# Kernel optimization log

Hardware: AMD Instinct MI355X
Metric: run time of the kernel (lower is better)

## Reference

```python
import jax, jax.numpy as jnp
from jax import lax
import numpy as np

H = W = 224
N = H * W
T = 25          # landscape sample points
K_MAX = 2       # number of landscapes
M_PTS = 64      # max persistence-diagram points kept (top persistence)
OUT_F = 50
CHUNK = 512     # pixels per DTM chunk


def _make_offsets(m0):
    # static, sorted-by-distance local window covering >= m0 fraction of mass for near-uniform weights
    r = int(np.ceil(np.sqrt(m0 * N / np.pi) * 1.3))
    dy, dx = np.meshgrid(np.arange(-r, r + 1), np.arange(-r, r + 1), indexing="ij")
    d2 = (dy * dy + dx * dx).astype(np.float32).ravel()
    o = np.argsort(d2, kind="stable")
    return jnp.asarray(dy.ravel()[o]), jnp.asarray(dx.ravel()[o]), jnp.asarray(d2[o]), r

_OFF = {m0: _make_offsets(m0) for m0 in (0.05, 0.2)}


def _dtm(w_img, m0):
    """Weighted distance-to-measure on the unit-spacing 224x224 grid.
    dtm(x)^2 = (1/(m0*W)) * sum of w_j * d_j^2 over nearest grid points until cumulative
    weight reaches m0*W (partial weight on the crossing point). Offsets are pre-sorted by
    distance (identical for every pixel), so no per-pixel sort is needed."""
    dy, dx, d2, r = _OFF[m0]
    B = w_img.shape[0]
    wp = jnp.pad(w_img, ((0, 0), (r, r), (r, r)))
    thr = m0 * w_img.sum(axis=(1, 2))                      # (B,)
    pix = jnp.arange(N).reshape(N // CHUNK, CHUNK)

    def body(p):
        y = p // W + r
        x = p % W + r
        vals = wp[:, y[:, None] + dy[None, :], x[:, None] + dx[None, :]]  # (B,C,O)
        c = jnp.cumsum(vals, axis=-1)
        used = jnp.minimum(jnp.maximum(thr[:, None, None] - (c - vals), 0.0), vals)
        return jnp.einsum("bco,o->bc", used, d2) / thr[:, None]

    dtm2 = lax.map(jax.checkpoint(body), pix)              # (n_chunks, B, CHUNK)
    return jnp.sqrt(jnp.maximum(dtm2.transpose(1, 0, 2).reshape(B, N), 0.0))


def _h0_pairs_np(f_batch):
    """0-dim persistent homology (sublevel filtration, 4-connectivity) via union-find.
    Returns indices of birth/death pixels so birth/death VALUES can be gathered
    differentiably in jax (PLLay-style gradients)."""
    f_batch = np.asarray(f_batch)
    B = f_batch.shape[0]
    b_idx = np.zeros((B, M_PTS), np.int32)
    d_idx = np.zeros((B, M_PTS), np.int32)
    mask = np.zeros((B, M_PTS), np.bool_)
    for bb in range(B):
        f = f_batch[bb]
        order = np.argsort(f, kind="stable")
        parent = np.full(N, -1, np.int64)
        pairs = []
        for i in order:
            i = int(i)
            parent[i] = i
            y, x = divmod(i, W)
            nbs = []
            if y > 0: nbs.append(i - W)
            if y < H - 1: nbs.append(i + W)
            if x > 0: nbs.append(i - 1)
            if x < W - 1: nbs.append(i + 1)
            for nb in nbs:
                if parent[nb] < 0:
                    continue
                ri = i
                while parent[ri] != ri:
                    parent[ri] = parent[parent[ri]]; ri = parent[ri]
                rn = nb
                while parent[rn] != rn:
                    parent[rn] = parent[parent[rn]]; rn = parent[rn]
                if ri == rn:
                    continue
                if f[ri] <= f[rn]:
                    elder, young = ri, rn
                else:
                    elder, young = rn, ri
                pairs.append((young, i))   # elder rule: younger component dies here
                parent[young] = elder
        pairs.append((int(np.argmin(f)), int(np.argmax(f))))  # essential class
        pa = np.asarray(pairs, np.int64)
        pers = f[pa[:, 1]] - f[pa[:, 0]]
        keep = np.argsort(-pers)[:M_PTS]
        k = len(keep)
        b_idx[bb, :k] = pa[keep, 0]
        d_idx[bb, :k] = pa[keep, 1]
        mask[bb, :k] = pers[keep] > 0
    return b_idx, d_idx, mask


def _topo_layer(x_img, m0, tseq, gw, gb):
    # AdTopoLayer: DTM -> H0 persistence diagram -> persistence landscapes at tseq -> Linear
    dt = _dtm(x_img, m0)                                   # (B, N)
    B = dt.shape[0]
    shapes = (jax.ShapeDtypeStruct((B, M_PTS), np.int32),
              jax.ShapeDtypeStruct((B, M_PTS), np.int32),
              jax.ShapeDtypeStruct((B, M_PTS), np.bool_))
    b_idx, d_idx, mask = jax.pure_callback(_h0_pairs_np, shapes, lax.stop_gradient(dt))
    birth = jnp.take_along_axis(dt, b_idx, axis=1)         # differentiable gather
    death = jnp.take_along_axis(dt, d_idx, axis=1)
    death = jnp.where(mask, death, birth)                  # invalid slots -> zero tent
    t = tseq[None, None, :]                                # (1,1,T)
    tents = jnp.maximum(jnp.minimum(t - birth[:, :, None], death[:, :, None] - t), 0.0)
    lam, _ = lax.top_k(tents.transpose(0, 2, 1), K_MAX)    # (B,T,K): k-th largest tents
    feat = lam.transpose(0, 2, 1).reshape(B, K_MAX * T)    # (B,50)
    return feat @ gw.T + gb


def _forward(input, params):
    xs = []
    for m0, g in ((0.05, "1"), (0.2, "2")):
        for c in range(3):
            n = "t" + g + str(c + 1)
            xs.append(_topo_layer(input[:, c], m0, params[n + "_tseq"], params[n + "_w"], params[n + "_b"]))
    x = jnp.concatenate(xs, axis=-1)                       # (B, 300)
    signal = jnp.abs(lax.stop_gradient(x)).sum(axis=0)     # (300,) detached signal
    output = jax.nn.relu(x) @ params["fc_w"].T + params["fc_b"]
    return output, signal


def setup_inputs():
    key = jax.random.key(0)
    ks = jax.random.split(key, 8)
    B = 2
    inp = {"input": jax.random.uniform(ks[0], (B, 3, H, W), jnp.float32)}
    centers = {"1": 20.0, "2": 40.0}   # typical DTM value ranges for m0=0.05 / 0.2
    i = 1
    for g in ("1", "2"):
        for c in ("1", "2", "3"):
            n = "t" + g + c
            kk = jax.random.fold_in(ks[1], i)
            inp[n + "_tseq"] = jnp.linspace(centers[g] - 15.0, centers[g] + 15.0, T).astype(jnp.float32)
            inp[n + "_w"] = 0.1 * jax.random.normal(kk, (OUT_F, K_MAX * T), jnp.float32)
            inp[n + "_b"] = jnp.zeros((OUT_F,), jnp.float32)
            i += 1
    inp["fc_w"] = 0.1 * jax.random.normal(ks[2], (7, 6 * OUT_F), jnp.float32)
    inp["fc_b"] = jnp.zeros((7,), jnp.float32)
    return inp


def reference(input, t11_tseq, t11_w, t11_b, t12_tseq, t12_w, t12_b, t13_tseq, t13_w, t13_b, t21_tseq, t21_w, t21_b, t22_tseq, t22_w, t22_b, t23_tseq, t23_w, t23_b, fc_w, fc_b):
    params = dict(t11_tseq=t11_tseq, t11_w=t11_w, t11_b=t11_b,
                  t12_tseq=t12_tseq, t12_w=t12_w, t12_b=t12_b,
                  t13_tseq=t13_tseq, t13_w=t13_w, t13_b=t13_b,
                  t21_tseq=t21_tseq, t21_w=t21_w, t21_b=t21_b,
                  t22_tseq=t22_tseq, t22_w=t22_w, t22_b=t22_b,
                  t23_tseq=t23_tseq, t23_w=t23_w, t23_b=t23_b,
                  fc_w=fc_w, fc_b=fc_b)
    return _forward(input, params)
```

## Files before the change

### kernel.cpp

```cpp
#include <hip/hip_runtime.h>
#include <stdint.h>

#define HWDIM 224
#define NPIX (HWDIM*HWDIM)
#define NFIELD 12
#define TT 25

#define R1v 37
#define PW1v (HWDIM + 2*R1v)
#define R2v 74
#define PW2v (HWDIM + 2*R2v)

#define HSIZE 16384
#define FCAP 4096
#define RHASH 4096
#define DON 36

typedef unsigned long long u64;

struct LayerParams {
    const float* tseq[6];
    const float* gw[6];
    const float* gb[6];
};

constexpr size_t alup(size_t x) { return (x + 255) & ~(size_t)255; }
constexpr size_t SZPA = (size_t)6*PW1v*(PW1v+1)*4;
constexpr size_t SZPB = (size_t)6*PW2v*(PW2v+1)*4;
constexpr size_t OFF_SUMS = 0;
constexpr size_t OFF_P0A = alup(OFF_SUMS + 8*4);
constexpr size_t OFF_PZA = alup(OFF_P0A + SZPA);
constexpr size_t OFF_P0B = alup(OFF_PZA + 2*SZPA);
constexpr size_t OFF_PZB = alup(OFF_P0B + SZPB);
constexpr size_t OFF_DT   = alup(OFF_PZB + 2*SZPB);
constexpr size_t OFF_PAR  = alup(OFF_DT   + (size_t)NFIELD*NPIX*4);
constexpr size_t OFF_HP   = alup(OFF_PAR  + (size_t)NFIELD*NPIX*2);
constexpr size_t OFF_HB   = alup(OFF_HP   + (size_t)NFIELD*HSIZE*8);
constexpr size_t OFF_GMM  = OFF_HB + (size_t)NFIELD*HSIZE*8;
constexpr size_t OFF_X    = alup(OFF_GMM + 256);


__global__ __launch_bounds__(64) void k_prefix(const float* __restrict__ inp,
        float* __restrict__ p0a, float2* __restrict__ pza,
        float* __restrict__ p0b, float2* __restrict__ pzb) {
    int bidx = blockIdx.x;
    const int tot0 = 6 * PW1v;
    int g = (bidx >= tot0);
    int rem = g ? (bidx - tot0) : bidx;
    const int PW = g ? PW2v : PW1v, R = g ? R2v : R1v, C = PW + 1;
    int img = rem / PW, row = rem % PW;
    float* P0 = (g ? p0b : p0a) + ((size_t)img*PW + row) * C;
    float2* PZ = (g ? pzb : pza) + ((size_t)img*PW + row) * C;
    int iy = row - R;
    bool rowok = ((unsigned)iy < HWDIM);
    const float* src = inp + (size_t)img*NPIX + (size_t)(rowok ? iy : 0)*HWDIM;
    const int lane = threadIdx.x;
    if (lane == 0) { P0[0] = 0.f; PZ[0] = make_float2(0.f, 0.f); }
    float c0 = 0.f, c1 = 0.f, c2 = 0.f;
    for (int i = 0; i < 6; ++i) {
        int k = i*64 + lane;
        float v = 0.f;
        if (k < PW && rowok) { int ix = k - R; if ((unsigned)ix < HWDIM) v = src[ix]; }
        float xd = (float)k;
        float w0 = v, w1 = v*xd, w2 = v*xd*xd;
        #pragma unroll
        for (int off = 1; off < 64; off <<= 1) {
            float t0 = __shfl_up(w0, off), t1 = __shfl_up(w1, off), t2 = __shfl_up(w2, off);
            if (lane >= off) { w0 += t0; w1 += t1; w2 += t2; }
        }
        if (k < PW) {
            P0[k+1] = c0 + w0;
            PZ[k+1] = make_float2(c1 + w1, c2 + w2);
        }
        c0 += __shfl(w0, 63); c1 += __shfl(w1, 63); c2 += __shfl(w2, 63);
    }
}

__global__ __launch_bounds__(256) void k_sums2(const float* __restrict__ p0a,
        float* __restrict__ sums) {
    int img = blockIdx.x;
    __shared__ float red[256];
    float s = 0.f;
    const int C = PW1v + 1;
    for (int r = threadIdx.x; r < PW1v; r += 256)
        s += p0a[((size_t)img*PW1v + r)*C + PW1v];
    red[threadIdx.x] = s; __syncthreads();
    for (int w = 128; w > 0; w >>= 1) {
        if (threadIdx.x < w) red[threadIdx.x] += red[threadIdx.x + w];
        __syncthreads();
    }
    if (threadIdx.x == 0) sums[img] = red[0];
}

__device__ __forceinline__ int k_init_exact(int X, int R) {
    int K = (int)sqrtf((float)X) + 1;
    if (K > R) K = R;
    while (K > 0 && K*K > X) --K;
    return K;
}

__device__ __forceinline__ float dmass1(int X, const float* __restrict__ P0, int bidx,
        int C, int R) {
    float m = 0.f;
    int K = 0;
    if (X >= 0) {
        K = k_init_exact(X, R);
        m = P0[bidx+K+1] - P0[bidx-K];
    }
    int t = X - 1, step = 3;
    const float* __restrict__ Pu = P0 - C;
    const float* __restrict__ Pd = P0 + C;
    for (int dyy = 1; dyy <= R; ++dyy) {
        if (__all(t < 0)) break;
        if (t >= 0) {
            while (K*K > t) --K;
            int A = bidx + K + 1, B = bidx - K;
            m += (Pu[A] - Pu[B]) + (Pd[A] - Pd[B]);
        }
        t -= step; step += 2; Pu -= C; Pd += C;
    }
    return m;
}

__global__ __launch_bounds__(256) void k_dtm(const float* __restrict__ sums,
        const float* __restrict__ p0a, const float2* __restrict__ pza,
        const float* __restrict__ p0b, const float2* __restrict__ pzb,
        float* __restrict__ dt) {
    const int xcd = blockIdx.x & 7, slot = blockIdx.x >> 3;
    int f, blk;
    if (xcd < 6) {
        if (slot < 196)            { f = 6 + xcd; blk = slot; }
        else if (slot < 196 + DON) { f = xcd; blk = (196 - DON) + (slot - 196); }
        else return;
    } else {
        const int per = 196 - DON;
        if (slot >= 3*per) return;
        int q = slot / per;
        f = (xcd - 6)*3 + q; blk = slot - q*per;
    }
    const int layer = f >> 1, b = f & 1;
    const int g = layer / 3, c = layer % 3;
    const int img = b*3 + c;
    const int R = g ? R2v : R1v, PW = g ? PW2v : PW1v, C = PW + 1;
    const int R2 = 2*R*R;
    const float thr = (g ? 0.2f : 0.05f) * sums[img];
    const float* __restrict__ P0 = (g ? p0b : p0a) + (size_t)img*PW*C;
    const float2* __restrict__ PZ = (g ? pzb : pza) + (size_t)img*PW*C;

    const int p = blk*256 + threadIdx.x;
    const int y = p / HWDIM, x = p % HWDIM;
    const int xc = x + R;
    const int bidx = (y + R)*C + xc;

    const int NP = g ? 7 : 6;
    const int WSTOP = g ? 86 : 43;
    int lo = 0, hi = R2 + 1;
    for (int it = 0; it < NP; ++it) {
        int X = (lo + hi) >> 1;
        float m = dmass1(X, P0, bidx, C, R);
        if (m >= thr) hi = X; else lo = X + 1;
    }
    for (int rit = 0; rit < 14; ++rit) {
        bool act = (hi == R2 + 1) ? (lo < hi) : (hi - lo > WSTOP);
        if (__all(!act)) break;
        int X = act ? ((lo + hi) >> 1) : -1;
        float m = dmass1(X, P0, bidx, C, R);
        if (X >= 0) { if (m >= thr) hi = X; else lo = X + 1; }
    }
    const bool nr = (hi == R2 + 1);
    const int  Dst = nr ? lo : ((lo + hi) >> 1);
    const bool cross = nr ? (lo <= R2) : true;
    const int  Xin = cross ? (Dst - 1) : R2;

    float m_in = 0.f, ws = 0.f;
    const float c2n = -2.f * (float)xc;
    const int xc2i = xc * xc;
    int K = 0;
    if (Xin >= 0) {
        K = k_init_exact(Xin, R);
        int A = bidx+K+1, B = bidx-K;
        float s0 = P0[A] - P0[B]; float2 zA = PZ[A], zB = PZ[B];
        m_in += s0; ws += fmaf((float)xc2i, s0, fmaf(c2n, zA.x - zB.x, zA.y - zB.y));
    }
    {
        int t = Xin - 1, step = 3, d2 = 1;
        const float* __restrict__ Pu = P0 - C;
        const float* __restrict__ Pd = P0 + C;
        const float2* __restrict__ Zu = PZ - C;
        const float2* __restrict__ Zd = PZ + C;
        for (int dyy = 1; dyy <= R; ++dyy) {
            if (__all(t < 0)) break;
            if (t >= 0) {
                while (K*K > t) --K;
                int A = bidx+K+1, B = bidx-K;
                float c1 = (float)(d2 + xc2i);
                { float s0 = Pu[A]-Pu[B]; float2 zA = Zu[A], zB = Zu[B];
                  m_in += s0; ws += fmaf(c1, s0, fmaf(c2n, zA.x - zB.x, zA.y - zB.y)); }
                { float s0 = Pd[A]-Pd[B]; float2 zA = Zd[A], zB = Zd[B];
                  m_in += s0; ws += fmaf(c1, s0, fmaf(c2n, zA.x - zB.x, zA.y - zB.y)); }
            }
            t -= step; d2 += step; step += 2;
            Pu -= C; Pd += C; Zu -= C; Zd += C;
        }
    }
    float s = cross ? (ws + (float)Dst * (thr - m_in)) : ws;
    float d = sqrtf(fmaxf(s / thr, 0.f));
    dt[(size_t)f*NPIX + p] = d;
}

__global__ __launch_bounds__(256) void k_desc(const float* __restrict__ dt,
        unsigned short* __restrict__ par, u64* __restrict__ gmm) {
    const int f = blockIdx.y;
    const int p = blockIdx.x*256 + threadIdx.x;
    const float* __restrict__ dtf = dt + (size_t)f*NPIX;
    float dc = dtf[p];
    u64 kc = ((u64)__float_as_uint(dc) << 32) | (unsigned)p;
    u64 best = kc; int bi = p;
    const int y = p / HWDIM, x = p % HWDIM;
    if (y > 0)        { float v = dtf[p - HWDIM]; u64 t = ((u64)__float_as_uint(v)<<32)|(unsigned)(p-HWDIM); if (t < best) { best = t; bi = p-HWDIM; } }
    if (y < HWDIM-1)  { float v = dtf[p + HWDIM]; u64 t = ((u64)__float_as_uint(v)<<32)|(unsigned)(p+HWDIM); if (t < best) { best = t; bi = p+HWDIM; } }
    if (x > 0)        { float v = dtf[p - 1];     u64 t = ((u64)__float_as_uint(v)<<32)|(unsigned)(p-1);     if (t < best) { best = t; bi = p-1; } }
    if (x < HWDIM-1)  { float v = dtf[p + 1];     u64 t = ((u64)__float_as_uint(v)<<32)|(unsigned)(p+1);     if (t < best) { best = t; bi = p+1; } }
    par[(size_t)f*NPIX + p] = (unsigned short)bi;
    __shared__ u64 rmin[256], rmax[256];
    u64 mk = ((u64)__float_as_uint(dc) << 32) | (unsigned)(0xFFFF - p);
    rmin[threadIdx.x] = kc; rmax[threadIdx.x] = mk;
    __syncthreads();
    for (int w = 128; w > 0; w >>= 1) {
        if (threadIdx.x < w) {
            if (rmin[threadIdx.x + w] < rmin[threadIdx.x]) rmin[threadIdx.x] = rmin[threadIdx.x + w];
            if (rmax[threadIdx.x + w] > rmax[threadIdx.x]) rmax[threadIdx.x] = rmax[threadIdx.x + w];
        }
        __syncthreads();
    }
    if (threadIdx.x == 0) {
        atomicMin(&gmm[f*2 + 0], rmin[0]);
        atomicMin(&gmm[f*2 + 1], ~rmax[0]);
    }
}

__device__ inline unsigned hash64(u64 x) {
    x ^= x >> 33; x *= 0xff51afd7ed558ccdULL;
    x ^= x >> 33; x *= 0xc4ceb9fe1a85ec53ULL;
    x ^= x >> 33;
    return (unsigned)x;
}

struct FinSh {
    u64 ek[FCAP];
    unsigned int epk[FCAP];
    unsigned int eab[FCAP];
    unsigned short eru[FCAP];
    int rhk[RHASH];
    short ufp[RHASH];
    float rdt[RHASH];
    unsigned int pyd[FCAP];
    float ppr[FCAP];
};

__device__ __forceinline__ void bitonic_n(u64* ek, int tid, int n, int bst) {
    for (int k = 2; k <= n; k <<= 1) {
        for (int j = k >> 1; j > 0; j >>= 1) {
            for (int i = tid; i < n; i += bst) {
                int ixj = i ^ j;
                if (ixj > i) {
                    u64 a = ek[i], b = ek[ixj];
                    if (((i & k) == 0) ? (a > b) : (a < b)) { ek[i] = b; ek[ixj] = a; }
                }
            }
            __syncthreads();
        }
    }
}

__global__ __launch_bounds__(1024) void k_fused(const float* __restrict__ dt,
        const unsigned short* __restrict__ parg, const u64* __restrict__ gmm,
        u64* __restrict__ hpair, u64* __restrict__ hbest,
        LayerParams lp, float* __restrict__ xbuf) {
    const int xcd = blockIdx.x & 7, slot = blockIdx.x >> 3;
    int f;
    if (xcd < 6) { if (slot != 0) return; f = 6 + xcd; }
    else f = (xcd - 6)*3 + slot;
    const int layer = f >> 1, bb = f & 1;
    const int tid = threadIdx.x; const int bs = 1024;
    const float* dtf = dt + (size_t)f*NPIX;
    u64* hp = hpair + (size_t)f*HSIZE;
    u64* hb = hbest + (size_t)f*HSIZE;

    __shared__ union U {
        unsigned short par[NPIX];
        FinSh fin;
    } sh;
    __shared__ float birth[64], death[64], featsh[2*TT];
    __shared__ int spec_a[64], spec_b[64];
    __shared__ u64 spec_e[64];
    __shared__ int cnt_s, pc_s;
    __shared__ int gmin_s, gmax_s; __shared__ float gminf_s, gmaxf_s;

    {
        const unsigned* src = (const unsigned*)(parg + (size_t)f*NPIX);
        unsigned* dst = (unsigned*)sh.par;
        for (int i = tid; i < NPIX/2; i += bs) dst[i] = src[i];
    }
    if (tid == 0) {
        u64 g0v = gmm[f*2 + 0];
        u64 g1v = ~gmm[f*2 + 1];
        gmin_s = (int)(unsigned)(g0v & 0xFFFFFFFFu);
        gminf_s = __uint_as_float((unsigned)(g0v >> 32));
        gmax_s = 0xFFFF - (int)(g1v & 0xFFFFu);
        gmaxf_s = __uint_as_float((unsigned)(g1v >> 32));
        cnt_s = 0; pc_s = 0;
    }
    __syncthreads();
    for (int pass = 0; pass < 6; ++pass) {
        for (int p = tid; p < NPIX; p += bs) sh.par[p] = sh.par[sh.par[p]];
        __syncthreads();
    }
    for (int p = tid; p < NPIX; p += bs) {
        int a = sh.par[p];
        int n = sh.par[a];
        while (n != a) { a = n; n = sh.par[a]; }
        sh.par[p] = (unsigned short)a;
    }
    __syncthreads();
    for (int p = tid; p < NPIX; p += bs) {
        const int rp = sh.par[p];
        const int y = p / HWDIM, x = p % HWDIM;
        const float dp = dtf[p];
        #pragma unroll
        for (int e = 0; e < 2; ++e) {
            int q;
            if (e == 0) { if (x >= HWDIM-1) continue; q = p + 1; }
            else        { if (y >= HWDIM-1) continue; q = p + HWDIM; }
            int rq = sh.par[q];
            if (rq == rp) continue;
            float dq = dtf[q];
            bool pdies = (dp > dq) || (dp == dq && p > q);
            u64 ekv = pdies
                ? (((u64)__float_as_uint(dp) << 32) | ((u64)(unsigned)p << 16) | (unsigned)rp)
                : (((u64)__float_as_uint(dq) << 32) | ((u64)(unsigned)q << 16) | (unsigned)rq);
            int ra = min(rp, rq), rb = max(rp, rq);
            u64 pk = ((u64)(unsigned)ra << 32) | (unsigned)rb;
            unsigned h = hash64(pk) & (HSIZE - 1);
            for (int probe = 0; probe < HSIZE; ++probe) {
                u64 old = atomicCAS(&hp[h], ~0ull, pk);
                if (old == ~0ull || old == pk) { atomicMin(&hb[h], ekv); break; }
                h = (h + 1) & (HSIZE - 1);
            }
        }
    }
    __syncthreads();
    for (int i = tid; i < RHASH; i += bs) sh.fin.rhk[i] = -1;
    __syncthreads();
    for (int i = tid; i < HSIZE; i += bs) {
        u64 pk = hp[i];
        if (pk != ~0ull) {
            int slot2 = atomicAdd(&cnt_s, 1);
            if (slot2 < FCAP) {
                u64 e = hb[i];
                unsigned u = (unsigned)((e >> 16) & 0xFFFFu);
                unsigned ru = (unsigned)(e & 0xFFFFu);
                sh.fin.ek[slot2] = (e & 0xFFFFFFFF00000000ull) | ((u64)u << 16) | (unsigned)slot2;
                int ra = (int)(pk >> 32), rb = (int)(pk & 0xFFFFFFFFu);
                sh.fin.epk[slot2] = ((unsigned)ra << 16) | (unsigned)rb;
                sh.fin.eru[slot2] = (unsigned short)ru;
                #pragma unroll
                for (int pass = 0; pass < 2; ++pass) {
                    int r = pass ? rb : ra;
                    unsigned h = ((unsigned)r * 2654435761u) & (RHASH - 1);
                    for (int pr = 0; pr < RHASH; ++pr) {
                        int old = atomicCAS(&sh.fin.rhk[h], -1, r);
                        if (old == -1 || old == r) break;
                        h = (h + 1) & (RHASH - 1);
                    }
                }
            }
        }
    }
    __syncthreads();
    int cnt = min(cnt_s, FCAP);
    int n1 = 64; while (n1 < cnt) n1 <<= 1;
    for (int s2 = tid; s2 < cnt; s2 += bs) {
        unsigned pk2 = sh.fin.epk[s2];
        int ra = (int)(pk2 >> 16), rb = (int)(pk2 & 0xFFFFu);
        int ru = sh.fin.eru[s2];
        int rv = (ru == ra) ? rb : ra;
        int su = -1, sv = -1;
        { unsigned h = ((unsigned)ru * 2654435761u) & (RHASH - 1);
          for (int pr = 0; pr < RHASH; ++pr) { int v = sh.fin.rhk[h]; if (v == ru) { su = (int)h; break; } if (v == -1) break; h = (h + 1) & (RHASH - 1); } }
        { unsigned h = ((unsigned)rv * 2654435761u) & (RHASH - 1);
          for (int pr = 0; pr < RHASH; ++pr) { int v = sh.fin.rhk[h]; if (v == rv) { sv = (int)h; break; } if (v == -1) break; h = (h + 1) & (RHASH - 1); } }
        sh.fin.eab[s2] = ((unsigned)su << 16) | (unsigned)(sv & 0xFFFF);
    }
    for (int i = cnt + tid; i < n1; i += bs) sh.fin.ek[i] = ~0ull;
    for (int s2 = tid; s2 < RHASH; s2 += bs) {
        sh.fin.ufp[s2] = (short)s2;
        int r = sh.fin.rhk[s2];
        sh.fin.rdt[s2] = (r >= 0) ? dtf[r] : 0.f;
    }
    __syncthreads();

    bitonic_n(sh.fin.ek, tid, n1, bs);

    if (tid < 64) {
        int pc = 0;
        for (int base = 0; base < cnt; base += 64) {
            int i = base + tid;
            int sa = -1, sb = -1; u64 e = ~0ull;
            if (i < cnt) {
                e = sh.fin.ek[i];
                int idx = (int)(e & 0xFFFFu);
                unsigned ab = sh.fin.eab[idx];
                sa = (int)(ab >> 16); sb = (int)(ab & 0xFFFFu);
                if (sa != 0xFFFF && sb != 0xFFFF) {
                    while (sh.fin.ufp[sa] != sa) { short g2 = sh.fin.ufp[sh.fin.ufp[sa]]; sh.fin.ufp[sa] = g2; sa = g2; }
                    while (sh.fin.ufp[sb] != sb) { short g2 = sh.fin.ufp[sh.fin.ufp[sb]]; sh.fin.ufp[sb] = g2; sb = g2; }
                    if (sa == sb) sa = -1;
                } else { sa = -1; }
            }
            spec_a[tid] = sa; spec_b[tid] = sb; spec_e[tid] = e;
            if (tid == 0) {
                int lim = min(64, cnt - base);
                for (int j = 0; j < lim; ++j) {
                    int sa2 = spec_a[j];
                    if (sa2 < 0) continue;
                    int sb2 = spec_b[j];
                    u64 e2 = spec_e[j];
                    while (sh.fin.ufp[sa2] != sa2) { short g2 = sh.fin.ufp[sh.fin.ufp[sa2]]; sh.fin.ufp[sa2] = g2; sa2 = g2; }
                    while (sh.fin.ufp[sb2] != sb2) { short g2 = sh.fin.ufp[sh.fin.ufp[sb2]]; sh.fin.ufp[sb2] = g2; sb2 = g2; }
                    if (sa2 == sb2) continue;
                    float fa = sh.fin.rdt[sa2], fb = sh.fin.rdt[sb2];
                    int elder, young;
                    if (fa <= fb) { elder = sa2; young = sb2; } else { elder = sb2; young = sa2; }
                    sh.fin.ufp[young] = (short)elder;
                    float pers = __uint_as_float((unsigned)(e2 >> 32)) - sh.fin.rdt[young];
                    if (pers > 0.f && pc < FCAP - 1) {
                        int u = (int)((e2 >> 16) & 0xFFFFu);
                        sh.fin.pyd[pc] = ((unsigned)sh.fin.rhk[young] << 16) | (unsigned)u;
                        sh.fin.ppr[pc] = pers; ++pc;
                    }
                }
            }
        }
        if (tid == 0) {
            sh.fin.pyd[pc] = ((unsigned)gmin_s << 16) | (unsigned)gmax_s;
            sh.fin.ppr[pc] = gmaxf_s - gminf_s; ++pc;
            pc_s = pc;
        }
    }
    __syncthreads();
    const int pc = pc_s;
    int n2 = 64; while (n2 < pc) n2 <<= 1;

    for (int i = tid; i < n2; i += bs) {
        if (i < pc && sh.fin.ppr[i] > 0.f)
            sh.fin.ek[i] = ((u64)(0xFFFFFFFFu - __float_as_uint(sh.fin.ppr[i])) << 32) | (unsigned)i;
        else sh.fin.ek[i] = ~0ull;
    }
    __syncthreads();
    bitonic_n(sh.fin.ek, tid, n2, bs);
    if (tid < 64) {
        u64 e = sh.fin.ek[tid];
        int bpix = 0, dpix = 0, msk = 0;
        if (e != ~0ull) {
            int i = (int)(e & 0xFFFFFFFFu);
            unsigned pd2 = sh.fin.pyd[i];
            bpix = (int)(pd2 >> 16); dpix = (int)(pd2 & 0xFFFFu); msk = 1;
        }
        float bv = dtf[bpix];
        float dv = msk ? dtf[dpix] : bv;
        birth[tid] = bv; death[tid] = dv;
    }
    __syncthreads();
    if (tid < TT) {
        float t = lp.tseq[layer][tid];
        float m1 = 0.f, m2 = 0.f;
        for (int m = 0; m < 64; ++m) {
            float v = fmaxf(fminf(t - birth[m], death[m] - t), 0.f);
            if (v > m1) { m2 = m1; m1 = v; } else if (v > m2) m2 = v;
        }
        featsh[tid] = m1; featsh[TT + tid] = m2;
    }
    __syncthreads();
    if (tid < 50) {
        const float* w = lp.gw[layer] + tid * 50;
        float acc = lp.gb[layer][tid];
        #pragma unroll
        for (int j = 0; j < 50; ++j) acc = fmaf(featsh[j], w[j], acc);
        xbuf[bb*300 + layer*50 + tid] = acc;
    }
}

__global__ __launch_bounds__(512) void k_final(const float* __restrict__ x, const float* __restrict__ fcw,
        const float* __restrict__ fcb, float* __restrict__ out) {
    __shared__ float rl[2][300];
    const int tid = threadIdx.x;
    if (tid < 300) {
        float a0 = x[tid], a1 = x[300 + tid];
        out[14 + tid] = fabsf(a0) + fabsf(a1);
        rl[0][tid] = fmaxf(a0, 0.f);
        rl[1][tid] = fmaxf(a1, 0.f);
    }
    __syncthreads();
    if (tid < 14) {
        int b = tid / 7, i = tid % 7;
        float acc = fcb[i];
        const float* w = fcw + i * 300;
        for (int j = 0; j < 300; ++j) acc = fmaf(rl[b][j], w[j], acc);
        out[b*7 + i] = acc;
    }
}

extern "C" void kernel_launch(void* const* d_in, const int* in_sizes, int n_in,
                              void* d_out, int out_size, void* d_ws, size_t ws_size,
                              hipStream_t stream) {
    (void)in_sizes; (void)n_in; (void)out_size; (void)ws_size;
    const float* inp = (const float*)d_in[0];
    LayerParams lp;
    for (int l = 0; l < 6; ++l) {
        lp.tseq[l] = (const float*)d_in[1 + 3*l];
        lp.gw[l]   = (const float*)d_in[2 + 3*l];
        lp.gb[l]   = (const float*)d_in[3 + 3*l];
    }
    const float* fcw = (const float*)d_in[19];
    const float* fcb = (const float*)d_in[20];

    char* w = (char*)d_ws;
    float* sums = (float*)(w + OFF_SUMS);
    float* p0a = (float*)(w + OFF_P0A);
    float2* pza = (float2*)(w + OFF_PZA);
    float* p0b = (float*)(w + OFF_P0B);
    float2* pzb = (float2*)(w + OFF_PZB);
    float* dt = (float*)(w + OFF_DT);
    unsigned short* par = (unsigned short*)(w + OFF_PAR);
    u64* hp = (u64*)(w + OFF_HP);
    u64* hb = (u64*)(w + OFF_HB);
    u64* gmm = (u64*)(w + OFF_GMM);
    float* xbuf = (float*)(w + OFF_X);

    const int prefRows = 6*PW1v + 6*PW2v;
    hipLaunchKernelGGL(k_prefix, dim3(prefRows), dim3(64), 0, stream,
                       inp, p0a, pza, p0b, pzb);
    hipLaunchKernelGGL(k_sums2, dim3(6), dim3(256), 0, stream, p0a, sums);
    hipMemsetAsync(hp, 0xFF, (size_t)2*NFIELD*HSIZE*8 + 256, stream);
    const int maxslot = 3 * (196 - DON);
    hipLaunchKernelGGL(k_dtm, dim3(8 * maxslot), dim3(256), 0, stream,
                       sums, p0a, pza, p0b, pzb, dt);
    hipLaunchKernelGGL(k_desc, dim3(NPIX/256, NFIELD), dim3(256), 0, stream, dt, par, gmm);
    hipLaunchKernelGGL(k_fused, dim3(24), dim3(1024), 0, stream,
                       dt, par, gmm, hp, hb, lp, xbuf);
    hipLaunchKernelGGL(k_final, dim3(1), dim3(512), 0, stream, xbuf, fcw, fcb, (float*)d_out);
}
```

Before: 721.7 us.

## Split fused persistence kernel into root, edge and finish kernels; shrink DTM blocks

The single 12-block fused kernel is split in three: root compression (one block per field), edge hashing across a full grid of 256-thread blocks, and a finish kernel that consumes the hash tables. This spreads the global-atomic edge phase over many CUs instead of 12 blocks. The DTM kernel also moves to 64-thread blocks with rescaled XCD slot mapping for finer load balance. The cost is extra kernel launches and a global round-trip of the root array.

```diff
diff --git a/kernel.cpp b/kernel.cpp
--- a/kernel.cpp
+++ b/kernel.cpp
@@ -14,7 +14,8 @@
 #define HSIZE 16384
 #define FCAP 4096
 #define RHASH 4096
-#define DON 36
+#define DON64 144
+#define BPF 784
 
 typedef unsigned long long u64;
 
@@ -122,18 +123,18 @@
     return m;
 }
 
-__global__ __launch_bounds__(256) void k_dtm(const float* __restrict__ sums,
+__global__ __launch_bounds__(64) void k_dtm(const float* __restrict__ sums,
         const float* __restrict__ p0a, const float2* __restrict__ pza,
         const float* __restrict__ p0b, const float2* __restrict__ pzb,
         float* __restrict__ dt) {
     const int xcd = blockIdx.x & 7, slot = blockIdx.x >> 3;
     int f, blk;
     if (xcd < 6) {
-        if (slot < 196)            { f = 6 + xcd; blk = slot; }
-        else if (slot < 196 + DON) { f = xcd; blk = (196 - DON) + (slot - 196); }
+        if (slot < BPF)              { f = 6 + xcd; blk = slot; }
+        else if (slot < BPF + DON64) { f = xcd; blk = slot - DON64; }
         else return;
     } else {
-        const int per = 196 - DON;
+        const int per = BPF - DON64;
         if (slot >= 3*per) return;
         int q = slot / per;
         f = (xcd - 6)*3 + q; blk = slot - q*per;
@@ -147,7 +148,7 @@
     const float* __restrict__ P0 = (g ? p0b : p0a) + (size_t)img*PW*C;
     const float2* __restrict__ PZ = (g ? pzb : pza) + (size_t)img*PW*C;
 
-    const int p = blk*256 + threadIdx.x;
+    const int p = blk*64 + threadIdx.x;
     const int y = p / HWDIM, x = p % HWDIM;
     const int xc = x + R;
     const int bidx = (y + R)*C + xc;
@@ -239,6 +240,34 @@
     }
 }
 
+__global__ __launch_bounds__(1024) void k_root(unsigned short* __restrict__ parg) {
+    const int f = blockIdx.x;
+    const int tid = threadIdx.x; const int bs = 1024;
+    __shared__ unsigned short par[NPIX];
+    {
+        const unsigned* src = (const unsigned*)(parg + (size_t)f*NPIX);
+        unsigned* dst = (unsigned*)par;
+        for (int i = tid; i < NPIX/2; i += bs) dst[i] = src[i];
+    }
+    __syncthreads();
+    for (int pass = 0; pass < 6; ++pass) {
+        for (int p = tid; p < NPIX; p += bs) par[p] = par[par[p]];
+        __syncthreads();
+    }
+    for (int p = tid; p < NPIX; p += bs) {
+        int a = par[p];
+        int n = par[a];
+        while (n != a) { a = n; n = par[a]; }
+        par[p] = (unsigned short)a;
+    }
+    __syncthreads();
+    {
+        const unsigned* src = (const unsigned*)par;
+        unsigned* dst = (unsigned*)(parg + (size_t)f*NPIX);
+        for (int i = tid; i < NPIX/2; i += bs) dst[i] = src[i];
+    }
+}
+
 __device__ inline unsigned hash64(u64 x) {
     x ^= x >> 33; x *= 0xff51afd7ed558ccdULL;
     x ^= x >> 33; x *= 0xc4ceb9fe1a85ec53ULL;
@@ -246,17 +275,40 @@
     return (unsigned)x;
 }
 
-struct FinSh {
-    u64 ek[FCAP];
-    unsigned int epk[FCAP];
-    unsigned int eab[FCAP];
-    unsigned short eru[FCAP];
-    int rhk[RHASH];
-    short ufp[RHASH];
-    float rdt[RHASH];
-    unsigned int pyd[FCAP];
-    float ppr[FCAP];
-};
+__global__ __launch_bounds__(256) void k_edges(const float* __restrict__ dt,
+        const unsigned short* __restrict__ parg,
+        u64* __restrict__ hpair, u64* __restrict__ hbest) {
+    const int f = blockIdx.y;
+    const int p = blockIdx.x*256 + threadIdx.x;
+    const float* __restrict__ dtf = dt + (size_t)f*NPIX;
+    const unsigned short* __restrict__ par = parg + (size_t)f*NPIX;
+    u64* hp = hpair + (size_t)f*HSIZE;
+    u64* hb = hbest + (size_t)f*HSIZE;
+    const int rp = par[p];
+    const int y = p / HWDIM, x = p % HWDIM;
+    const float dp = dtf[p];
+    #pragma unroll
+    for (int e = 0; e < 2; ++e) {
+        int q;
+        if (e == 0) { if (x >= HWDIM-1) continue; q = p + 1; }
+        else        { if (y >= HWDIM-1) continue; q = p + HWDIM; }
+        int rq = par[q];
+        if (rq == rp) continue;
+        float dq = dtf[q];
+        bool pdies = (dp > dq) || (dp == dq && p > q);
+        u64 ekv = pdies
+            ? (((u64)__float_as_uint(dp) << 32) | ((u64)(unsigned)p << 16) | (unsigned)rp)
+            : (((u64)__float_as_uint(dq) << 32) | ((u64)(unsigned)q << 16) | (unsigned)rq);
+        int ra = min(rp, rq), rb = max(rp, rq);
+        u64 pk = ((u64)(unsigned)ra << 32) | (unsigned)rb;
+        unsigned h = hash64(pk) & (HSIZE - 1);
+        for (int probe = 0; probe < HSIZE; ++probe) {
+            u64 old = atomicCAS(&hp[h], ~0ull, pk);
+            if (old == ~0ull || old == pk) { atomicMin(&hb[h], ekv); break; }
+            h = (h + 1) & (HSIZE - 1);
+        }
+    }
+}
 
 __device__ __forceinline__ void bitonic_n(u64* ek, int tid, int n, int bst) {
     for (int k = 2; k <= n; k <<= 1) {
@@ -273,35 +325,32 @@
     }
 }
 
-__global__ __launch_bounds__(1024) void k_fused(const float* __restrict__ dt,
-        const unsigned short* __restrict__ parg, const u64* __restrict__ gmm,
-        u64* __restrict__ hpair, u64* __restrict__ hbest,
+__global__ __launch_bounds__(1024) void k_finish(const float* __restrict__ dt,
+        const u64* __restrict__ gmm,
+        const u64* __restrict__ hpair, const u64* __restrict__ hbest,
         LayerParams lp, float* __restrict__ xbuf) {
-    const int xcd = blockIdx.x & 7, slot = blockIdx.x >> 3;
-    int f;
-    if (xcd < 6) { if (slot != 0) return; f = 6 + xcd; }
-    else f = (xcd - 6)*3 + slot;
+    const int f = blockIdx.x;
     const int layer = f >> 1, bb = f & 1;
     const int tid = threadIdx.x; const int bs = 1024;
     const float* dtf = dt + (size_t)f*NPIX;
-    u64* hp = hpair + (size_t)f*HSIZE;
-    u64* hb = hbest + (size_t)f*HSIZE;
-
-    __shared__ union U {
-        unsigned short par[NPIX];
-        FinSh fin;
-    } sh;
+    const u64* hp = hpair + (size_t)f*HSIZE;
+    const u64* hb = hbest + (size_t)f*HSIZE;
+
+    __shared__ u64 ek[FCAP];
+    __shared__ unsigned int epk[FCAP];
+    __shared__ unsigned int eab[FCAP];
+    __shared__ unsigned short eru[FCAP];
+    __shared__ int rhk[RHASH];
+    __shared__ short ufp[RHASH];
+    __shared__ float rdt[RHASH];
+    __shared__ unsigned int pyd[FCAP];
+    __shared__ float ppr[FCAP];
     __shared__ float birth[64], death[64], featsh[2*TT];
     __shared__ int spec_a[64], spec_b[64];
     __shared__ u64 spec_e[64];
     __shared__ int cnt_s, pc_s;
     __shared__ int gmin_s, gmax_s; __shared__ float gminf_s, gmaxf_s;
 
-    {
-        const unsigned* src = (const unsigned*)(parg + (size_t)f*NPIX);
-        unsigned* dst = (unsigned*)sh.par;
-        for (int i = tid; i < NPIX/2; i += bs) dst[i] = src[i];
-    }
     if (tid == 0) {
         u64 g0v = gmm[f*2 + 0];
         u64 g1v = ~gmm[f*2 + 1];
@@ -311,46 +360,7 @@
         gmaxf_s = __uint_as_float((unsigned)(g1v >> 32));
         cnt_s = 0; pc_s = 0;
     }
-    __syncthreads();
-    for (int pass = 0; pass < 6; ++pass) {
-        for (int p = tid; p < NPIX; p += bs) sh.par[p] = sh.par[sh.par[p]];
-        __syncthreads();
-    }
-    for (int p = tid; p < NPIX; p += bs) {
-        int a = sh.par[p];
-        int n = sh.par[a];
-        while (n != a) { a = n; n = sh.par[a]; }
-        sh.par[p] = (unsigned short)a;
-    }
-    __syncthreads();
-    for (int p = tid; p < NPIX; p += bs) {
-        const int rp = sh.par[p];
-        const int y = p / HWDIM, x = p % HWDIM;
-        const float dp = dtf[p];
-        #pragma unroll
-        for (int e = 0; e < 2; ++e) {
-            int q;
-            if (e == 0) { if (x >= HWDIM-1) continue; q = p + 1; }
-            else        { if (y >= HWDIM-1) continue; q = p + HWDIM; }
-            int rq = sh.par[q];
-            if (rq == rp) continue;
-            float dq = dtf[q];
-            bool pdies = (dp > dq) || (dp == dq && p > q);
-            u64 ekv = pdies
-                ? (((u64)__float_as_uint(dp) << 32) | ((u64)(unsigned)p << 16) | (unsigned)rp)
-                : (((u64)__float_as_uint(dq) << 32) | ((u64)(unsigned)q << 16) | (unsigned)rq);
-            int ra = min(rp, rq), rb = max(rp, rq);
-            u64 pk = ((u64)(unsigned)ra << 32) | (unsigned)rb;
-            unsigned h = hash64(pk) & (HSIZE - 1);
-            for (int probe = 0; probe < HSIZE; ++probe) {
-                u64 old = atomicCAS(&hp[h], ~0ull, pk);
-                if (old == ~0ull || old == pk) { atomicMin(&hb[h], ekv); break; }
-                h = (h + 1) & (HSIZE - 1);
-            }
-        }
-    }
-    __syncthreads();
-    for (int i = tid; i < RHASH; i += bs) sh.fin.rhk[i] = -1;
+    for (int i = tid; i < RHASH; i += bs) rhk[i] = -1;
     __syncthreads();
     for (int i = tid; i < HSIZE; i += bs) {
         u64 pk = hp[i];
@@ -360,16 +370,16 @@
                 u64 e = hb[i];
                 unsigned u = (unsigned)((e >> 16) & 0xFFFFu);
                 unsigned ru = (unsigned)(e & 0xFFFFu);
-                sh.fin.ek[slot2] = (e & 0xFFFFFFFF00000000ull) | ((u64)u << 16) | (unsigned)slot2;
+                ek[slot2] = (e & 0xFFFFFFFF00000000ull) | ((u64)u << 16) | (unsigned)slot2;
                 int ra = (int)(pk >> 32), rb = (int)(pk & 0xFFFFFFFFu);
-                sh.fin.epk[slot2] = ((unsigned)ra << 16) | (unsigned)rb;
-                sh.fin.eru[slot2] = (unsigned short)ru;
+                epk[slot2] = ((unsigned)ra << 16) | (unsigned)rb;
+                eru[slot2] = (unsigned short)ru;
                 #pragma unroll
                 for (int pass = 0; pass < 2; ++pass) {
                     int r = pass ? rb : ra;
                     unsigned h = ((unsigned)r * 2654435761u) & (RHASH - 1);
                     for (int pr = 0; pr < RHASH; ++pr) {
-                        int old = atomicCAS(&sh.fin.rhk[h], -1, r);
+                        int old = atomicCAS(&rhk[h], -1, r);
                         if (old == -1 || old == r) break;
                         h = (h + 1) & (RHASH - 1);
                     }
@@ -381,26 +391,26 @@
     int cnt = min(cnt_s, FCAP);
     int n1 = 64; while (n1 < cnt) n1 <<= 1;
     for (int s2 = tid; s2 < cnt; s2 += bs) {
-        unsigned pk2 = sh.fin.epk[s2];
+        unsigned pk2 = epk[s2];
         int ra = (int)(pk2 >> 16), rb = (int)(pk2 & 0xFFFFu);
-        int ru = sh.fin.eru[s2];
+        int ru = eru[s2];
         int rv = (ru == ra) ? rb : ra;
         int su = -1, sv = -1;
         { unsigned h = ((unsigned)ru * 2654435761u) & (RHASH - 1);
-          for (int pr = 0; pr < RHASH; ++pr) { int v = sh.fin.rhk[h]; if (v == ru) { su = (int)h; break; } if (v == -1) break; h = (h + 1) & (RHASH - 1); } }
+          for (int pr = 0; pr < RHASH; ++pr) { int v = rhk[h]; if (v == ru) { su = (int)h; break; } if (v == -1) break; h = (h + 1) & (RHASH - 1); } }
         { unsigned h = ((unsigned)rv * 2654435761u) & (RHASH - 1);
-          for (int pr = 0; pr < RHASH; ++pr) { int v = sh.fin.rhk[h]; if (v == rv) { sv = (int)h; break; } if (v == -1) break; h = (h + 1) & (RHASH - 1); } }
-        sh.fin.eab[s2] = ((unsigned)su << 16) | (unsigned)(sv & 0xFFFF);
-    }
-    for (int i = cnt + tid; i < n1; i += bs) sh.fin.ek[i] = ~0ull;
+          for (int pr = 0; pr < RHASH; ++pr) { int v = rhk[h]; if (v == rv) { sv = (int)h; break; } if (v == -1) break; h = (h + 1) & (RHASH - 1); } }
+        eab[s2] = ((unsigned)su << 16) | (unsigned)(sv & 0xFFFF);
+    }
+    for (int i = cnt + tid; i < n1; i += bs) ek[i] = ~0ull;
     for (int s2 = tid; s2 < RHASH; s2 += bs) {
-        sh.fin.ufp[s2] = (short)s2;
-        int r = sh.fin.rhk[s2];
-        sh.fin.rdt[s2] = (r >= 0) ? dtf[r] : 0.f;
-    }
-    __syncthreads();
-
-    bitonic_n(sh.fin.ek, tid, n1, bs);
+        ufp[s2] = (short)s2;
+        int r = rhk[s2];
+        rdt[s2] = (r >= 0) ? dtf[r] : 0.f;
+    }
+    __syncthreads();
+
+    bitonic_n(ek, tid, n1, bs);
 
     if (tid < 64) {
         int pc = 0;
@@ -408,13 +418,13 @@
             int i = base + tid;
             int sa = -1, sb = -1; u64 e = ~0ull;
             if (i < cnt) {
-                e = sh.fin.ek[i];
+                e = ek[i];
                 int idx = (int)(e & 0xFFFFu);
-                unsigned ab = sh.fin.eab[idx];
+                unsigned ab = eab[idx];
                 sa = (int)(ab >> 16); sb = (int)(ab & 0xFFFFu);
                 if (sa != 0xFFFF && sb != 0xFFFF) {
-                    while (sh.fin.ufp[sa] != sa) { short g2 = sh.fin.ufp[sh.fin.ufp[sa]]; sh.fin.ufp[sa] = g2; sa = g2; }
-                    while (sh.fin.ufp[sb] != sb) { short g2 = sh.fin.ufp[sh.fin.ufp[sb]]; sh.fin.ufp[sb] = g2; sb = g2; }
+                    while (ufp[sa] != sa) { short g2 = ufp[ufp[sa]]; ufp[sa] = g2; sa = g2; }
+                    while (ufp[sb] != sb) { short g2 = ufp[ufp[sb]]; ufp[sb] = g2; sb = g2; }
                     if (sa == sb) sa = -1;
                 } else { sa = -1; }
             }
@@ -426,25 +436,25 @@
                     if (sa2 < 0) continue;
                     int sb2 = spec_b[j];
                     u64 e2 = spec_e[j];
-                    while (sh.fin.ufp[sa2] != sa2) { short g2 = sh.fin.ufp[sh.fin.ufp[sa2]]; sh.fin.ufp[sa2] = g2; sa2 = g2; }
-                    while (sh.fin.ufp[sb2] != sb2) { short g2 = sh.fin.ufp[sh.fin.ufp[sb2]]; sh.fin.ufp[sb2] = g2; sb2 = g2; }
+                    while (ufp[sa2] != sa2) { short g2 = ufp[ufp[sa2]]; ufp[sa2] = g2; sa2 = g2; }
+                    while (ufp[sb2] != sb2) { short g2 = ufp[ufp[sb2]]; ufp[sb2] = g2; sb2 = g2; }
                     if (sa2 == sb2) continue;
-                    float fa = sh.fin.rdt[sa2], fb = sh.fin.rdt[sb2];
+                    float fa = rdt[sa2], fb = rdt[sb2];
                     int elder, young;
                     if (fa <= fb) { elder = sa2; young = sb2; } else { elder = sb2; young = sa2; }
-                    sh.fin.ufp[young] = (short)elder;
-                    float pers = __uint_as_float((unsigned)(e2 >> 32)) - sh.fin.rdt[young];
+                    ufp[young] = (short)elder;
+                    float pers = __uint_as_float((unsigned)(e2 >> 32)) - rdt[young];
                     if (pers > 0.f && pc < FCAP - 1) {
                         int u = (int)((e2 >> 16) & 0xFFFFu);
-                        sh.fin.pyd[pc] = ((unsigned)sh.fin.rhk[young] << 16) | (unsigned)u;
-                        sh.fin.ppr[pc] = pers; ++pc;
+                        pyd[pc] = ((unsigned)rhk[young] << 16) | (unsigned)u;
+                        ppr[pc] = pers; ++pc;
                     }
                 }
             }
         }
         if (tid == 0) {
-            sh.fin.pyd[pc] = ((unsigned)gmin_s << 16) | (unsigned)gmax_s;
-            sh.fin.ppr[pc] = gmaxf_s - gminf_s; ++pc;
+            pyd[pc] = ((unsigned)gmin_s << 16) | (unsigned)gmax_s;
+            ppr[pc] = gmaxf_s - gminf_s; ++pc;
             pc_s = pc;
         }
     }
@@ -453,18 +463,18 @@
     int n2 = 64; while (n2 < pc) n2 <<= 1;
 
     for (int i = tid; i < n2; i += bs) {
-        if (i < pc && sh.fin.ppr[i] > 0.f)
-            sh.fin.ek[i] = ((u64)(0xFFFFFFFFu - __float_as_uint(sh.fin.ppr[i])) << 32) | (unsigned)i;
-        else sh.fin.ek[i] = ~0ull;
-    }
-    __syncthreads();
-    bitonic_n(sh.fin.ek, tid, n2, bs);
+        if (i < pc && ppr[i] > 0.f)
+            ek[i] = ((u64)(0xFFFFFFFFu - __float_as_uint(ppr[i])) << 32) | (unsigned)i;
+        else ek[i] = ~0ull;
+    }
+    __syncthreads();
+    bitonic_n(ek, tid, n2, bs);
     if (tid < 64) {
-        u64 e = sh.fin.ek[tid];
+        u64 e = ek[tid];
         int bpix = 0, dpix = 0, msk = 0;
         if (e != ~0ull) {
             int i = (int)(e & 0xFFFFFFFFu);
-            unsigned pd2 = sh.fin.pyd[i];
+            unsigned pd2 = pyd[i];
             bpix = (int)(pd2 >> 16); dpix = (int)(pd2 & 0xFFFFu); msk = 1;
         }
         float bv = dtf[bpix];
@@ -543,11 +553,12 @@
                        inp, p0a, pza, p0b, pzb);
     hipLaunchKernelGGL(k_sums2, dim3(6), dim3(256), 0, stream, p0a, sums);
     hipMemsetAsync(hp, 0xFF, (size_t)2*NFIELD*HSIZE*8 + 256, stream);
-    const int maxslot = 3 * (196 - DON);
-    hipLaunchKernelGGL(k_dtm, dim3(8 * maxslot), dim3(256), 0, stream,
+    const int maxslot = 3 * (BPF - DON64);
+    hipLaunchKernelGGL(k_dtm, dim3(8 * maxslot), dim3(64), 0, stream,
                        sums, p0a, pza, p0b, pzb, dt);
     hipLaunchKernelGGL(k_desc, dim3(NPIX/256, NFIELD), dim3(256), 0, stream, dt, par, gmm);
-    hipLaunchKernelGGL(k_fused, dim3(24), dim3(1024), 0, stream,
-                       dt, par, gmm, hp, hb, lp, xbuf);
+    hipLaunchKernelGGL(k_root, dim3(NFIELD), dim3(1024), 0, stream, par);
+    hipLaunchKernelGGL(k_edges, dim3(NPIX/256, NFIELD), dim3(256), 0, stream, dt, par, hp, hb);
+    hipLaunchKernelGGL(k_finish, dim3(NFIELD), dim3(1024), 0, stream, dt, gmm, hp, hb, lp, xbuf);
     hipLaunchKernelGGL(k_final, dim3(1), dim3(512), 0, stream, xbuf, fcw, fcb, (float*)d_out);
 }
```

Result: faster. 655.6 us, median of 2 (-9.2%).
